# Optimization experiments

Hardware: AMD Instinct MI355X
Metric: run time of the kernel (lower is better)

Reference implementation:

```python
import jax, jax.numpy as jnp
import numpy as np

W = 801  # wavelength grid points
B = 16384  # batch of thickness stacks


def setup_inputs() -> dict:
    key = jax.random.key(0)
    k1, = jax.random.split(key, 1)
    # 7 physical film thicknesses in nm, uniform in [0, 200)
    d_phys = jax.random.uniform(k1, (B, 7), dtype=jnp.float32) * 200.0
    # wavelength grid in nm (docstring: spectrum length 801)
    lam = jnp.linspace(400.0, 800.0, W, dtype=jnp.float32)
    # material refractive indices (module default fallbacks, complex n + ik)
    n_Si = jnp.full((W,), 4.0 + 0.0j, dtype=jnp.complex64)
    n_SiO2 = jnp.full((W,), 1.46 + 0.0j, dtype=jnp.complex64)
    n_Si3N4 = jnp.full((W,), 2.0 + 0.0j, dtype=jnp.complex64)
    return {"d_phys": d_phys, "n_Si": n_Si, "n_SiO2": n_SiO2,
            "n_Si3N4": n_Si3N4, "lam": lam}


def reference(d_phys, n_Si, n_SiO2, n_Si3N4, lam):
    # Transfer-matrix reflectometry for stack:
    # Air | SiO2 | Si3N4 | SiO2 | Si3N4 | SiO2 | Si3N4 | SiO2 | Si
    k0 = (2.0 * jnp.pi) / lam  # [W]
    b = d_phys.shape[0]
    n_Air = jnp.ones_like(n_Si)
    layers_n = [n_Air, n_SiO2, n_Si3N4, n_SiO2, n_Si3N4,
                n_SiO2, n_Si3N4, n_SiO2, n_Si]
    zeros = jnp.zeros((b, 1), dtype=d_phys.dtype)
    d_list = [zeros] + [d_phys[:, i:i + 1] for i in range(7)] + [zeros]

    M00 = jnp.ones((b, lam.shape[0]), dtype=jnp.complex64)
    M11 = jnp.ones_like(M00)
    M01 = jnp.zeros_like(M00)
    M10 = jnp.zeros_like(M00)

    N_curr = layers_n[0]
    n_layers = len(layers_n)
    for i in range(1, n_layers):  # fixed 8-step recurrence over interfaces
        N_next = layers_n[i]
        d_next = d_list[i]  # [b, 1] real
        sum_n = N_curr + N_next  # [W]
        sub_n = N_curr - N_next
        r = sub_n / sum_n            # Fresnel reflection coeff [W]
        inv_t = sum_n / (2.0 * N_curr)  # 1/transmission [W]
        m00 = (M00 + M01 * r) * inv_t
        m01 = (M00 * r + M01) * inv_t
        m10 = (M10 + M11 * r) * inv_t
        m11 = (M10 * r + M11) * inv_t
        M00, M01, M10, M11 = m00, m01, m10, m11
        if i < n_layers - 1:
            phi = k0[None, :] * N_next[None, :] * d_next.astype(jnp.complex64)  # [b, W]
            P = jnp.exp(-1j * phi)
            Pi = jnp.exp(1j * phi)
            M00 = M00 * P
            M01 = M01 * Pi
            M10 = M10 * P
            M11 = M11 * Pi
        N_curr = N_next

    r_final = M10 / M00
    R = jnp.abs(r_final) ** 2  # real reflectance spectrum [b, W]
    return R
```

## Files before the change

kernel.cpp:

```cpp
#include <hip/hip_runtime.h>

#define WPTS 801
#define ROWS 16
#define NT 256

struct c2 { float x, y; };

__device__ __forceinline__ c2 c_add(c2 a, c2 b) { return {a.x + b.x, a.y + b.y}; }
__device__ __forceinline__ c2 c_sub(c2 a, c2 b) { return {a.x - b.x, a.y - b.y}; }
__device__ __forceinline__ c2 c_div(c2 a, c2 b) {
    float inv = 1.0f / (b.x * b.x + b.y * b.y);
    return {(a.x * b.x + a.y * b.y) * inv, (a.y * b.x - a.x * b.y) * inv};
}

__global__ __launch_bounds__(NT)
void kla_tmm_kernel(const float* __restrict__ d_phys,
                    const float* __restrict__ nSi_f,
                    const float* __restrict__ nSiO2_f,
                    const float* __restrict__ nSi3N4_f,
                    const float* __restrict__ lam,
                    float* __restrict__ out,
                    int B)
{
    const int nRowBlks = (B + ROWS - 1) / ROWS;
    const int t = blockIdx.x * NT + threadIdx.x;
    if (t >= nRowBlks * WPTS) return;

    const int w = t % WPTS;
    const int row0 = (t / WPTS) * ROWS;
    const int nrows = min(ROWS, B - row0);

    const bool ilv = (nSiO2_f[1] == 0.0f);
    float nSx, nSy, nOx, nOy, nNx, nNy;
    if (ilv) {
        nSx = nSi_f[2 * w];    nSy = nSi_f[2 * w + 1];
        nOx = nSiO2_f[2 * w];  nOy = nSiO2_f[2 * w + 1];
        nNx = nSi3N4_f[2 * w]; nNy = nSi3N4_f[2 * w + 1];
    } else {
        nSx = nSi_f[w];    nSy = 0.0f;
        nOx = nSiO2_f[w];  nOy = 0.0f;
        nNx = nSi3N4_f[w]; nNy = 0.0f;
    }

    const float k0 = 6.28318530717958647692f / lam[w];

    const bool realn = (nOy == 0.0f) && (nNy == 0.0f) && (nSy == 0.0f);

    if (realn) {
        const float rAO  = (1.0f - nOx) / (1.0f + nOx);
        const float rON  = (nOx - nNx) / (nOx + nNx);
        const float rNO  = -rON;
        const float rOSi = (nOx - nSx) / (nOx + nSx);
        const float kO = k0 * nOx;
        const float kN = k0 * nNx;

        for (int rr = 0; rr < nrows; ++rr) {
            const int row = row0 + rr;
            const float* dd = d_phys + (size_t)row * 7;
            float d1 = dd[0], d2 = dd[1], d3 = dd[2], d4 = dd[3],
                  d5 = dd[4], d6 = dd[5], d7 = dd[6];

            float u0x = 1.0f, u0y = 0.0f, u1x = rOSi, u1y = 0.0f;

            #pragma unroll
            for (int i = 7; i >= 1; --i) {
                const float d = (i == 1) ? d1 : (i == 2) ? d2 : (i == 3) ? d3 :
                                (i == 4) ? d4 : (i == 5) ? d5 : (i == 6) ? d6 : d7;
                const float alpha = d * ((i & 1) ? kO : kN);
                float s, c;
                __sincosf(alpha, &s, &c);
                const float t0x = u0x * c + u0y * s;
                const float t0y = u0y * c - u0x * s;
                const float t1x = u1x * c - u1y * s;
                const float t1y = u1y * c + u1x * s;
                const float r = (i == 1) ? rAO : ((i & 1) ? rNO : rON);
                u0x = t0x + r * t1x;
                u0y = t0y + r * t1y;
                u1x = t1x + r * t0x;
                u1y = t1y + r * t0y;
            }
            out[(size_t)row * WPTS + w] =
                (u1x * u1x + u1y * u1y) / (u0x * u0x + u0y * u0y);
        }
    } else {
        const c2 nA = {1.0f, 0.0f};
        const c2 nO = {nOx, nOy}, nN = {nNx, nNy}, nS = {nSx, nSy};
        const c2 rAO  = c_div(c_sub(nA, nO), c_add(nA, nO));
        const c2 rON  = c_div(c_sub(nO, nN), c_add(nO, nN));
        const c2 rNO  = {-rON.x, -rON.y};
        const c2 rOSi = c_div(c_sub(nO, nS), c_add(nO, nS));
        const c2 kO = {k0 * nO.x, k0 * nO.y};
        const c2 kN = {k0 * nN.x, k0 * nN.y};

        for (int rr = 0; rr < nrows; ++rr) {
            const int row = row0 + rr;
            const float* dd = d_phys + (size_t)row * 7;

            c2 u0 = {1.0f, 0.0f};
            c2 u1 = rOSi;

            #pragma unroll
            for (int i = 7; i >= 1; --i) {
                const float d = dd[i - 1];
                const c2 kk = (i & 1) ? kO : kN;
                const float alpha = kk.x * d;
                const float beta  = kk.y * d;
                float s, c;
                __sincosf(alpha, &s, &c);
                const float ep = __expf(beta);
                const float em = __expf(-beta);

                c2 v;
                v.x = ep * (u0.x * c + u0.y * s);
                v.y = ep * (u0.y * c - u0.x * s);
                u0 = v;
                v.x = em * (u1.x * c - u1.y * s);
                v.y = em * (u1.y * c + u1.x * s);
                u1 = v;

                const c2 ri = (i == 1) ? rAO : ((i & 1) ? rNO : rON);
                c2 w0, w1;
                w0.x = u0.x + ri.x * u1.x - ri.y * u1.y;
                w0.y = u0.y + ri.x * u1.y + ri.y * u1.x;
                w1.x = u1.x + ri.x * u0.x - ri.y * u0.y;
                w1.y = u1.y + ri.x * u0.y + ri.y * u0.x;
                u0 = w0; u1 = w1;
            }

            out[(size_t)row * WPTS + w] =
                (u1.x * u1.x + u1.y * u1.y) / (u0.x * u0.x + u0.y * u0.y);
        }
    }
}

extern "C" void kernel_launch(void* const* d_in, const int* in_sizes, int n_in,
                              void* d_out, int out_size, void* d_ws, size_t ws_size,
                              hipStream_t stream) {
    const float* d_phys  = (const float*)d_in[0];
    const float* nSi     = (const float*)d_in[1];
    const float* nSiO2   = (const float*)d_in[2];
    const float* nSi3N4  = (const float*)d_in[3];
    const float* lam     = (const float*)d_in[4];
    float* out = (float*)d_out;

    const int B = in_sizes[0] / 7;
    const int nRowBlks = (B + ROWS - 1) / ROWS;
    const int nTasks = nRowBlks * WPTS;
    const int grid = (nTasks + NT - 1) / NT;

    kla_tmm_kernel<<<grid, NT, 0, stream>>>(
        d_phys, nSi, nSiO2, nSi3N4, lam, out, B);
}
```

Before: 48.55 us.

## Reformulate real-index TMM in normalized field basis with hardware sin/cos

Rewrites the real-index path to propagate fields in a (n·E, H)-style basis, so each interface becomes a single real scale factor instead of a Fresnel mixing step. Phases use the revolution-scaled hardware sin/cos builtins (d·n/λ, no 2π factor), and the reciprocal builtin replaces the divisions. Rows per thread drop from 16 to 4 with a fully unrolled row loop, which gives more threads and more instruction-level parallelism. The trade-off is reduced accuracy from the native approximate transcendentals and reciprocals, and partial row blocks fall back to the complex path.

```diff
diff --git a/kernel.cpp b/kernel.cpp
--- a/kernel.cpp
+++ b/kernel.cpp
@@ -1,14 +1,14 @@
 #include <hip/hip_runtime.h>
 
 #define WPTS 801
-#define ROWS 16
+#define ROWS 4
 #define NT 256
 
 struct c2 { float x, y; };
 
-__device__ __forceinline__ c2 c_add(c2 a, c2 b) { return {a.x + b.x, a.y + b.y}; }
-__device__ __forceinline__ c2 c_sub(c2 a, c2 b) { return {a.x - b.x, a.y - b.y}; }
-__device__ __forceinline__ c2 c_div(c2 a, c2 b) {
+__device__ __forceinline__ c2 c_addc(c2 a, c2 b) { return {a.x + b.x, a.y + b.y}; }
+__device__ __forceinline__ c2 c_subc(c2 a, c2 b) { return {a.x - b.x, a.y - b.y}; }
+__device__ __forceinline__ c2 c_divc(c2 a, c2 b) {
     float inv = 1.0f / (b.x * b.x + b.y * b.y);
     return {(a.x * b.x + a.y * b.y) * inv, (a.y * b.x - a.x * b.y) * inv};
 }
@@ -42,53 +42,55 @@
         nNx = nSi3N4_f[w]; nNy = 0.0f;
     }
 
-    const float k0 = 6.28318530717958647692f / lam[w];
-
     const bool realn = (nOy == 0.0f) && (nNy == 0.0f) && (nSy == 0.0f);
 
-    if (realn) {
-        const float rAO  = (1.0f - nOx) / (1.0f + nOx);
-        const float rON  = (nOx - nNx) / (nOx + nNx);
-        const float rNO  = -rON;
-        const float rOSi = (nOx - nSx) / (nOx + nSx);
-        const float kO = k0 * nOx;
-        const float kN = k0 * nNx;
+    if (realn && nrows == ROWS) {
+        const float rlam = __builtin_amdgcn_rcpf(lam[w]);
+        const float kOr = nOx * rlam;
+        const float kNr = nNx * rlam;
+        const float gAO = __builtin_amdgcn_rcpf(nOx);
+        const float gON = nOx * __builtin_amdgcn_rcpf(nNx);
+        const float gNO = nNx * gAO;
 
-        for (int rr = 0; rr < nrows; ++rr) {
-            const int row = row0 + rr;
-            const float* dd = d_phys + (size_t)row * 7;
-            float d1 = dd[0], d2 = dd[1], d3 = dd[2], d4 = dd[3],
-                  d5 = dd[4], d6 = dd[5], d7 = dd[6];
+        const float* base = d_phys + (size_t)row0 * 7;
+        float* orow = out + (size_t)row0 * WPTS + w;
 
-            float u0x = 1.0f, u0y = 0.0f, u1x = rOSi, u1y = 0.0f;
+        #pragma unroll
+        for (int rr = 0; rr < ROWS; ++rr) {
+            const float* dd = base + (size_t)rr * 7;
+            float v0x = nOx, v0y = 0.0f;
+            float v1x = nSx, v1y = 0.0f;
 
             #pragma unroll
             for (int i = 7; i >= 1; --i) {
-                const float d = (i == 1) ? d1 : (i == 2) ? d2 : (i == 3) ? d3 :
-                                (i == 4) ? d4 : (i == 5) ? d5 : (i == 6) ? d6 : d7;
-                const float alpha = d * ((i & 1) ? kO : kN);
-                float s, c;
-                __sincosf(alpha, &s, &c);
-                const float t0x = u0x * c + u0y * s;
-                const float t0y = u0y * c - u0x * s;
-                const float t1x = u1x * c - u1y * s;
-                const float t1y = u1y * c + u1x * s;
-                const float r = (i == 1) ? rAO : ((i & 1) ? rNO : rON);
-                u0x = t0x + r * t1x;
-                u0y = t0y + r * t1y;
-                u1x = t1x + r * t0x;
-                u1y = t1y + r * t0y;
+                const float nu = dd[i - 1] * ((i & 1) ? kOr : kNr);
+                const float s = __builtin_amdgcn_sinf(nu);
+                const float c = __builtin_amdgcn_cosf(nu);
+                const float w0x = v0x * c + v1y * s;
+                const float w0y = v0y * c - v1x * s;
+                const float w1x = v1x * c + v0y * s;
+                const float w1y = v1y * c - v0x * s;
+                const float g = (i == 1) ? gAO : ((i & 1) ? gNO : gON);
+                v0x = w0x * g;
+                v0y = w0y * g;
+                v1x = w1x;
+                v1y = w1y;
             }
-            out[(size_t)row * WPTS + w] =
-                (u1x * u1x + u1y * u1y) / (u0x * u0x + u0y * u0y);
+
+            const float ax = v0x - v1x, ay = v0y - v1y;
+            const float bx = v0x + v1x, by = v0y + v1y;
+            const float num = ax * ax + ay * ay;
+            const float den = bx * bx + by * by;
+            orow[(size_t)rr * WPTS] = num * __builtin_amdgcn_rcpf(den);
         }
     } else {
+        const float k0 = 6.28318530717958647692f / lam[w];
         const c2 nA = {1.0f, 0.0f};
         const c2 nO = {nOx, nOy}, nN = {nNx, nNy}, nS = {nSx, nSy};
-        const c2 rAO  = c_div(c_sub(nA, nO), c_add(nA, nO));
-        const c2 rON  = c_div(c_sub(nO, nN), c_add(nO, nN));
+        const c2 rAO  = c_divc(c_subc(nA, nO), c_addc(nA, nO));
+        const c2 rON  = c_divc(c_subc(nO, nN), c_addc(nO, nN));
         const c2 rNO  = {-rON.x, -rON.y};
-        const c2 rOSi = c_div(c_sub(nO, nS), c_add(nO, nS));
+        const c2 rOSi = c_divc(c_subc(nO, nS), c_addc(nO, nS));
         const c2 kO = {k0 * nO.x, k0 * nO.y};
         const c2 kN = {k0 * nN.x, k0 * nN.y};
 
```

Result: faster. 47.40 us (-2.4%).
